# Kernel optimization log

Measured on AMD Instinct MI355X. Metric: run time of the kernel, lower is better.

## Reference

```python
import jax, jax.numpy as jnp
import numpy as np

B, T, D, K = 4, 4096, 1024, 64


def setup_inputs() -> dict:
    key = jax.random.key(0)
    k1, k2, k3, k4 = jax.random.split(key, 4)
    x = jax.random.normal(k1, (B, T, D), dtype=jnp.float32)
    Wq = jax.random.normal(k2, (D, K), dtype=jnp.float32) * (D ** -0.5)
    Wk = jax.random.normal(k3, (D, K), dtype=jnp.float32) * (D ** -0.5)
    Wv = jax.random.normal(k4, (D, D), dtype=jnp.float32) * (D ** -0.5)
    return {"x": x, "Wq": Wq, "Wk": Wk, "Wv": Wv}


def reference(x, Wq, Wk, Wv):
    # x: (B,T,D); single-head causal self-attention with value dim = D
    Bx, Tx, Dx = x.shape
    head_size = Wq.shape[-1]
    q = jnp.einsum('btd,dk->btk', x, Wq)  # (B,T,K)
    k = jnp.einsum('btd,dk->btk', x, Wk)  # (B,T,K)
    v = jnp.einsum('btd,de->bte', x, Wv)  # (B,T,D)
    scores = jnp.einsum('bqk,bsk->bqs', q, k) * (head_size ** -0.5)  # (B,T,T)
    causal = jnp.tril(jnp.ones((Tx, Tx), dtype=bool))
    scores = jnp.where(causal[None, :, :], scores, -jnp.inf)
    attn = jax.nn.softmax(scores, axis=-1)
    return jnp.einsum('bqs,bsd->bqd', attn, v)  # (B,T,D)
```

## Files before the change

kernel.cpp:

```cpp
#include <hip/hip_runtime.h>
#include <hip/hip_bf16.h>

typedef __attribute__((ext_vector_type(8))) short bf16x8;
typedef __attribute__((ext_vector_type(4))) float f32x4;
typedef unsigned short u16;

#define MFMA16(a, b, c) __builtin_amdgcn_mfma_f32_16x16x32_bf16((a), (b), (c), 0, 0, 0)
#define GLLDS(gp, lp)                                                                  \
  __builtin_amdgcn_global_load_lds((const __attribute__((address_space(1))) unsigned int*)(gp), \
                                   (__attribute__((address_space(3))) unsigned int*)(lp), 16, 0, 0)

__device__ __forceinline__ float fexp2(float x) { return __builtin_amdgcn_exp2f(x); }

__device__ __forceinline__ u16 f2b(float f) {
  union { float f; unsigned u; } x; x.f = f;
  return (u16)((x.u + 0x7FFFu + ((x.u >> 16) & 1u)) >> 16);
}
__device__ __forceinline__ unsigned f2b_hw(float f) {
  union { __hip_bfloat16 h; u16 u; } c;
  c.h = __float2bfloat16(f);
  return (unsigned)c.u;
}

__global__ __launch_bounds__(256) void k_cvt(const float* __restrict__ in,
                                             u16* __restrict__ out, int n4) {
  int i = blockIdx.x * 256 + threadIdx.x;
  if (i >= n4) return;
  float4 v = ((const float4*)in)[i];
  u16 a = f2b(v.x), b = f2b(v.y), c = f2b(v.z), d = f2b(v.w);
  ((uint2*)out)[i] = make_uint2((unsigned)a | ((unsigned)b << 16),
                                (unsigned)c | ((unsigned)d << 16));
}

__global__ __launch_bounds__(256) void k_packT(const float* __restrict__ in,
                                               u16* __restrict__ out, int R, int C) {
  __shared__ float t[32][33];
  int r0 = blockIdx.x * 32, c0 = blockIdx.y * 32;
  int cx = threadIdx.x & 31, ry = threadIdx.x >> 5;
#pragma unroll
  for (int k = 0; k < 4; k++)
    t[ry + k * 8][cx] = in[(size_t)(r0 + ry + k * 8) * C + c0 + cx];
  __syncthreads();
#pragma unroll
  for (int k = 0; k < 4; k++)
    out[(size_t)(c0 + ry + k * 8) * R + r0 + cx] = f2b(t[cx][ry + k * 8]);
}

__global__ __launch_bounds__(256) void k_gemm_qk(const u16* __restrict__ xb,
                                                 const u16* __restrict__ wqt,
                                                 const u16* __restrict__ wkt,
                                                 u16* __restrict__ q, u16* __restrict__ kk) {
  int row0 = blockIdx.x * 64;
  int tid = threadIdx.x, w = tid >> 6, l = tid & 63, l15 = l & 15, lg = l >> 4;
  const u16* wt = (w < 2) ? wqt : wkt;
  int nbase = (w & 1) * 32;
  f32x4 acc[4][2];
#pragma unroll
  for (int mt = 0; mt < 4; mt++)
#pragma unroll
    for (int nt = 0; nt < 2; nt++) acc[mt][nt] = (f32x4){0.f, 0.f, 0.f, 0.f};

  for (int k0 = 0; k0 < 1024; k0 += 32) {
    bf16x8 bfr[2], afr[4];
#pragma unroll
    for (int nt = 0; nt < 2; nt++)
      bfr[nt] = *(const bf16x8*)&wt[(size_t)(nbase + nt * 16 + l15) * 1024 + k0 + lg * 8];
#pragma unroll
    for (int mt = 0; mt < 4; mt++)
      afr[mt] = *(const bf16x8*)&xb[(size_t)(row0 + mt * 16 + l15) * 1024 + k0 + lg * 8];
#pragma unroll
    for (int mt = 0; mt < 4; mt++)
#pragma unroll
      for (int nt = 0; nt < 2; nt++) acc[mt][nt] = MFMA16(afr[mt], bfr[nt], acc[mt][nt]);
  }
  if (w < 2) {
#pragma unroll
    for (int mt = 0; mt < 4; mt++)
#pragma unroll
      for (int nt = 0; nt < 2; nt++)
#pragma unroll
        for (int j = 0; j < 4; j++)
          q[(size_t)(row0 + mt * 16 + lg * 4 + j) * 64 + nbase + nt * 16 + l15] =
              f2b(acc[mt][nt][j] * 0.18033688f);
  } else {
#pragma unroll
    for (int mt = 0; mt < 4; mt++)
#pragma unroll
      for (int nt = 0; nt < 2; nt++)
#pragma unroll
        for (int j = 0; j < 4; j++) {
          int row = row0 + mt * 16 + lg * 4 + j;
          int c = (nbase + nt * 16 + l15) * 2;
          size_t off = (size_t)(row >> 6) * 8192 + (row & 63) * 128 + (c ^ ((row & 7) << 4));
          *(u16*)((char*)kk + off) = f2b(acc[mt][nt][j]);
        }
  }
}

__global__ __launch_bounds__(256) void k_gemm_v(const u16* __restrict__ xb,
                                                const u16* __restrict__ wvt,
                                                u16* __restrict__ vT) {
  int b = blockIdx.z;
  int d0 = blockIdx.y * 128;
  int s0 = blockIdx.x * 128;
  int tid = threadIdx.x, w = tid >> 6, l = tid & 63, l15 = l & 15, lg = l >> 4;
  int wd = (w & 1) * 64, wsn = (w >> 1) * 64;
  __shared__ __align__(16) char lds[32768];

  const u16* arow = wvt + (size_t)d0 * 1024;
  const u16* brow = xb + (size_t)(b * 4096 + s0) * 1024;

  auto stage = [&](int buf, int k0) {
    char* La = lds + buf * 16384;
    char* Lb = La + 8192;
#pragma unroll
    for (int i = 0; i < 2; i++) {
      int row = w * 32 + i * 16 + (l >> 2), kq = (l & 3) * 8;
      GLLDS(&arow[(size_t)row * 1024 + k0 + kq], La + (w * 2 + i) * 1024);
      GLLDS(&brow[(size_t)row * 1024 + k0 + kq], Lb + (w * 2 + i) * 1024);
    }
  };

  f32x4 acc[4][4];
#pragma unroll
  for (int mt = 0; mt < 4; mt++)
#pragma unroll
    for (int nt = 0; nt < 4; nt++) acc[mt][nt] = (f32x4){0.f, 0.f, 0.f, 0.f};

  stage(0, 0);
  __syncthreads();
  int buf = 0;
  for (int k = 0; k < 32; k++) {
    if (k < 31) stage(buf ^ 1, (k + 1) * 32);
    const char* La = lds + buf * 16384;
    const char* Lb = La + 8192;
    bf16x8 afr[4], bfr[4];
#pragma unroll
    for (int mt = 0; mt < 4; mt++)
      afr[mt] = *(const bf16x8*)(La + (wd + mt * 16 + l15) * 64 + lg * 16);
#pragma unroll
    for (int nt = 0; nt < 4; nt++)
      bfr[nt] = *(const bf16x8*)(Lb + (wsn + nt * 16 + l15) * 64 + lg * 16);
    __builtin_amdgcn_s_setprio(1);
#pragma unroll
    for (int mt = 0; mt < 4; mt++)
#pragma unroll
      for (int nt = 0; nt < 4; nt++) acc[mt][nt] = MFMA16(afr[mt], bfr[nt], acc[mt][nt]);
    __builtin_amdgcn_s_setprio(0);
    __syncthreads();
    buf ^= 1;
  }
#pragma unroll
  for (int mt = 0; mt < 4; mt++)
#pragma unroll
    for (int nt = 0; nt < 4; nt++)
#pragma unroll
      for (int j = 0; j < 4; j++) {
        int d = d0 + wd + mt * 16 + lg * 4 + j;
        int s = s0 + wsn + nt * 16 + l15;
        size_t off = ((size_t)(b * 64 + (s >> 6)) * 8 + (d >> 7)) * 16384 + (d & 127) * 128 +
                     (((s & 63) * 2) ^ ((d & 7) << 4));
        *(u16*)((char*)vT + off) = f2b(acc[mt][nt][j]);
      }
}

__global__ __launch_bounds__(512, 2) void k_attn(const u16* __restrict__ qw,
                                                 const u16* __restrict__ kws,
                                                 const u16* __restrict__ vts,
                                                 float* __restrict__ out) {
  int bid = blockIdx.x;
  int xcd = bid & 7, r = bid >> 3;
  int cmb = r & 1, q5 = r >> 1;
  int half = q5 >> 4, idx = q5 & 15;
  int p = half ? 31 - idx : idx;
  int g = xcd * 2 + cmb;
  int cpair = g & 3, b = g >> 2;
  int tid = threadIdx.x, w = tid >> 6, l = tid & 63, l15 = l & 15, lg = l >> 4;
  int sw = (l15 & 7) << 4;
  size_t tokb = (size_t)b * 4096;

  __shared__ __align__(16) char lds[66048];
  char* Pb = lds + 49152;
  float* scb = (float*)(lds + 65536);

  const short ob = (short)0x3F80;
  const bf16x8 ones = {ob, ob, ob, ob, ob, ob, ob, ob};
  const bf16x8 zf = {0, 0, 0, 0, 0, 0, 0, 0};

  auto stageV = [&](int t) {
    const char* vb = (const char*)vts + ((size_t)(b * 64 + t) * 8 + cpair * 2) * 16384;
    char* lv = lds + 16384;
#pragma unroll
    for (int i = 0; i < 4; i++) {
      int s = w * 4 + i;
      GLLDS(vb + s * 1024 + l * 16, lv + s * 1024);
    }
  };
  auto stageK = [&](int t, int bufi) {
    const char* kb = (const char*)kws + (size_t)(b * 64 + t) * 8192;
    GLLDS(kb + w * 1024 + l * 16, lds + bufi * 8192 + w * 1024);
  };

  int Q0 = p * 128;
  int ntb = (Q0 >> 6) + 2;
  int qsA = Q0 + w * 16;
  int qA = qsA + l15;
  int qsB = Q0 + (w & 3) * 32;
  int dhalf = w >> 2;

  bf16x8 qf[2];
#pragma unroll
  for (int ks = 0; ks < 2; ks++)
    qf[ks] = *(const bf16x8*)&qw[(tokb + qA) * 64 + ks * 32 + lg * 8];

  f32x4 acc[8][2], accl[2];
  float mrow = -1e30f;
#pragma unroll
  for (int mt = 0; mt < 8; mt++)
#pragma unroll
    for (int qt = 0; qt < 2; qt++) acc[mt][qt] = (f32x4){0.f, 0.f, 0.f, 0.f};
  accl[0] = (f32x4){0.f, 0.f, 0.f, 0.f};
  accl[1] = (f32x4){0.f, 0.f, 0.f, 0.f};

  stageK(0, 0);
  __syncthreads();
  int buf = 0;
  for (int t = 0; t < ntb; t++) {
    int s0 = t * 64;
    stageV(t);
    if (t + 1 < ntb) stageK(t + 1, buf ^ 1);
    if (s0 < qsA + 16) {
      const char* Kb = lds + buf * 8192;
      f32x4 sfr[4];
      __builtin_amdgcn_s_setprio(1);
#pragma unroll
      for (int nt = 0; nt < 4; nt++) {
        const char* kr = Kb + (nt * 16 + l15) * 128;
        bf16x8 kf0 = *(const bf16x8*)(kr + ((lg * 16) ^ sw));
        bf16x8 kf1 = *(const bf16x8*)(kr + ((64 + lg * 16) ^ sw));
        f32x4 z = (f32x4){0.f, 0.f, 0.f, 0.f};
        z = MFMA16(kf0, qf[0], z);
        sfr[nt] = MFMA16(kf1, qf[1], z);
      }
      __builtin_amdgcn_s_setprio(0);
      if (s0 + 63 > qsA) {
#pragma unroll
        for (int nt = 0; nt < 4; nt++)
#pragma unroll
          for (int j = 0; j < 4; j++)
            if (s0 + nt * 16 + lg * 4 + j > qA) sfr[nt][j] = -1e30f;
      }
      float pm = fmaxf(fmaxf(fmaxf(sfr[0][0], sfr[0][1]), fmaxf(sfr[0][2], sfr[0][3])),
                       fmaxf(fmaxf(sfr[1][0], sfr[1][1]), fmaxf(sfr[1][2], sfr[1][3])));
      pm = fmaxf(pm, fmaxf(fmaxf(fmaxf(sfr[2][0], sfr[2][1]), fmaxf(sfr[2][2], sfr[2][3])),
                           fmaxf(fmaxf(sfr[3][0], sfr[3][1]), fmaxf(sfr[3][2], sfr[3][3]))));
      pm = fmaxf(pm, __shfl_xor(pm, 16));
      pm = fmaxf(pm, __shfl_xor(pm, 32));
      float sc = 1.0f;
      if (__any(pm > mrow + 11.54f)) {
        float mn = fmaxf(mrow, pm);
        sc = fexp2(mrow - mn);
        mrow = mn;
      }
      int rq = w * 16 + l15;
      scb[rq] = sc;
      int rbase = rq * 128, sx = (rq & 7) << 4;
#pragma unroll
      for (int nt = 0; nt < 4; nt++) {
        unsigned lo = f2b_hw(fexp2(sfr[nt][0] - mrow)) |
                      (f2b_hw(fexp2(sfr[nt][1] - mrow)) << 16);
        unsigned hi2 = f2b_hw(fexp2(sfr[nt][2] - mrow)) |
                       (f2b_hw(fexp2(sfr[nt][3] - mrow)) << 16);
        int addr = (rbase + (nt * 16 + lg * 4) * 2) ^ sx;
        *(uint2*)(Pb + addr) = make_uint2(lo, hi2);
      }
    }
    __syncthreads();
    if (s0 < qsB + 32) {
      const char* Vb = lds + 16384 + dhalf * 16384;
      bool act0 = s0 < qsB + 16;
      int R0 = (w & 3) * 32 + l15;
      if (act0) {
        float sq0 = scb[R0];
        if (!__all(sq0 == 1.0f)) {
#pragma unroll
          for (int mt = 0; mt < 8; mt++) acc[mt][0] *= sq0;
          accl[0] *= sq0;
        }
      }
      {
        float sq1 = scb[R0 + 16];
        if (!__all(sq1 == 1.0f)) {
#pragma unroll
          for (int mt = 0; mt < 8; mt++) acc[mt][1] *= sq1;
          accl[1] *= sq1;
        }
      }
      bf16x8 pf00 = zf, pf01 = zf, pf10, pf11;
      if (act0) {
        int rx = (R0 & 7) << 4;
        pf00 = *(const bf16x8*)(Pb + ((R0 * 128 + lg * 16) ^ rx));
        pf01 = *(const bf16x8*)(Pb + ((R0 * 128 + 64 + lg * 16) ^ rx));
      }
      {
        int R1 = R0 + 16, rx = (R1 & 7) << 4;
        pf10 = *(const bf16x8*)(Pb + ((R1 * 128 + lg * 16) ^ rx));
        pf11 = *(const bf16x8*)(Pb + ((R1 * 128 + 64 + lg * 16) ^ rx));
      }
      __builtin_amdgcn_s_setprio(1);
      accl[0] = MFMA16(ones, pf00, accl[0]);
      accl[0] = MFMA16(ones, pf01, accl[0]);
      accl[1] = MFMA16(ones, pf10, accl[1]);
      accl[1] = MFMA16(ones, pf11, accl[1]);
#pragma unroll
      for (int mt = 0; mt < 8; mt++) {
        const char* vr = Vb + (mt * 16 + l15) * 128;
        bf16x8 va0 = *(const bf16x8*)(vr + ((lg * 16) ^ sw));
        bf16x8 va1 = *(const bf16x8*)(vr + ((64 + lg * 16) ^ sw));
        acc[mt][0] = MFMA16(va0, pf00, acc[mt][0]);
        acc[mt][0] = MFMA16(va1, pf01, acc[mt][0]);
        acc[mt][1] = MFMA16(va0, pf10, acc[mt][1]);
        acc[mt][1] = MFMA16(va1, pf11, acc[mt][1]);
      }
      __builtin_amdgcn_s_setprio(0);
    }
    __syncthreads();
    buf ^= 1;
  }
#pragma unroll
  for (int qt = 0; qt < 2; qt++) {
    float linv = 1.0f / accl[qt][0];
#pragma unroll
    for (int mt = 0; mt < 8; mt++) {
      f32x4 v = acc[mt][qt] * linv;
      size_t o = (tokb + qsB + qt * 16 + l15) * 1024 + cpair * 256 + dhalf * 128 +
                 mt * 16 + lg * 4;
      *(f32x4*)&out[o] = v;
    }
  }
}

extern "C" void kernel_launch(void* const* d_in, const int* in_sizes, int n_in,
                              void* d_out, int out_size, void* d_ws, size_t ws_size,
                              hipStream_t stream) {
  const float* x  = (const float*)d_in[0];
  const float* Wq = (const float*)d_in[1];
  const float* Wk = (const float*)d_in[2];
  const float* Wv = (const float*)d_in[3];
  float* out = (float*)d_out;
  char* ws = (char*)d_ws;
  u16* xb  = (u16*)(ws);
  u16* qw  = (u16*)(ws + 33554432);
  u16* kw  = (u16*)(ws + 35651584);
  u16* vT  = (u16*)(ws + 37748736);
  u16* wqt = (u16*)(ws + 71303168);
  u16* wkt = (u16*)(ws + 71434240);
  u16* wvt = (u16*)(ws + 71565312);

  k_cvt<<<16384, 256, 0, stream>>>(x, xb, 4194304);
  k_packT<<<dim3(32, 2), 256, 0, stream>>>(Wq, wqt, 1024, 64);
  k_packT<<<dim3(32, 2), 256, 0, stream>>>(Wk, wkt, 1024, 64);
  k_packT<<<dim3(32, 32), 256, 0, stream>>>(Wv, wvt, 1024, 1024);
  k_gemm_qk<<<256, 256, 0, stream>>>(xb, wqt, wkt, qw, kw);
  k_gemm_v<<<dim3(32, 8, 4), 256, 0, stream>>>(xb, wvt, vT);
  k_attn<<<512, 512, 0, stream>>>(qw, kw, vT, out);
}
```

Baseline: 218.0 us.

## Load K fragments directly to registers and track softmax row sums in registers

```diff
diff --git a/kernel.cpp b/kernel.cpp
--- a/kernel.cpp
+++ b/kernel.cpp
@@ -179,26 +179,20 @@
   int sw = (l15 & 7) << 4;
   size_t tokb = (size_t)b * 4096;
 
-  __shared__ __align__(16) char lds[66048];
-  char* Pb = lds + 49152;
-  float* scb = (float*)(lds + 65536);
-
-  const short ob = (short)0x3F80;
-  const bf16x8 ones = {ob, ob, ob, ob, ob, ob, ob, ob};
+  __shared__ __align__(16) char lds[50176];
+  char* Pb = lds + 32768;
+  float* scb = (float*)(lds + 49152);
+  float* lb = (float*)(lds + 49664);
+
   const bf16x8 zf = {0, 0, 0, 0, 0, 0, 0, 0};
 
   auto stageV = [&](int t) {
     const char* vb = (const char*)vts + ((size_t)(b * 64 + t) * 8 + cpair * 2) * 16384;
-    char* lv = lds + 16384;
 #pragma unroll
     for (int i = 0; i < 4; i++) {
       int s = w * 4 + i;
-      GLLDS(vb + s * 1024 + l * 16, lv + s * 1024);
-    }
-  };
-  auto stageK = [&](int t, int bufi) {
-    const char* kb = (const char*)kws + (size_t)(b * 64 + t) * 8192;
-    GLLDS(kb + w * 1024 + l * 16, lds + bufi * 8192 + w * 1024);
+      GLLDS(vb + s * 1024 + l * 16, lds + s * 1024);
+    }
   };
 
   int Q0 = p * 128;
@@ -213,36 +207,47 @@
   for (int ks = 0; ks < 2; ks++)
     qf[ks] = *(const bf16x8*)&qw[(tokb + qA) * 64 + ks * 32 + lg * 8];
 
-  f32x4 acc[8][2], accl[2];
-  float mrow = -1e30f;
+  bf16x8 kf[4][2];
+  {
+    const char* kb = (const char*)kws + (size_t)(b * 64) * 8192;
+#pragma unroll
+    for (int nt = 0; nt < 4; nt++) {
+      const char* kr = kb + (nt * 16 + l15) * 128;
+      kf[nt][0] = *(const bf16x8*)(kr + ((lg * 16) ^ sw));
+      kf[nt][1] = *(const bf16x8*)(kr + ((64 + lg * 16) ^ sw));
+    }
+  }
+
+  f32x4 acc[8][2];
+  float mrow = -1e30f, Lrun = 0.f;
 #pragma unroll
   for (int mt = 0; mt < 8; mt++)
 #pragma unroll
     for (int qt = 0; qt < 2; qt++) acc[mt][qt] = (f32x4){0.f, 0.f, 0.f, 0.f};
-  accl[0] = (f32x4){0.f, 0.f, 0.f, 0.f};
-  accl[1] = (f32x4){0.f, 0.f, 0.f, 0.f};
-
-  stageK(0, 0);
-  __syncthreads();
-  int buf = 0;
+
   for (int t = 0; t < ntb; t++) {
     int s0 = t * 64;
     stageV(t);
-    if (t + 1 < ntb) stageK(t + 1, buf ^ 1);
     if (s0 < qsA + 16) {
-      const char* Kb = lds + buf * 8192;
       f32x4 sfr[4];
       __builtin_amdgcn_s_setprio(1);
 #pragma unroll
       for (int nt = 0; nt < 4; nt++) {
-        const char* kr = Kb + (nt * 16 + l15) * 128;
-        bf16x8 kf0 = *(const bf16x8*)(kr + ((lg * 16) ^ sw));
-        bf16x8 kf1 = *(const bf16x8*)(kr + ((64 + lg * 16) ^ sw));
         f32x4 z = (f32x4){0.f, 0.f, 0.f, 0.f};
-        z = MFMA16(kf0, qf[0], z);
-        sfr[nt] = MFMA16(kf1, qf[1], z);
+        z = MFMA16(kf[nt][0], qf[0], z);
+        sfr[nt] = MFMA16(kf[nt][1], qf[1], z);
       }
       __builtin_amdgcn_s_setprio(0);
+      {
+        int tn = (t + 1 < ntb) ? t + 1 : t;
+        const char* kbn = (const char*)kws + (size_t)(b * 64 + tn) * 8192;
+#pragma unroll
+        for (int nt = 0; nt < 4; nt++) {
+          const char* kr = kbn + (nt * 16 + l15) * 128;
+          kf[nt][0] = *(const bf16x8*)(kr + ((lg * 16) ^ sw));
+          kf[nt][1] = *(const bf16x8*)(kr + ((64 + lg * 16) ^ sw));
+        }
+      }
       if (s0 + 63 > qsA) {
 #pragma unroll
         for (int nt = 0; nt < 4; nt++)
@@ -265,19 +270,26 @@
       int rq = w * 16 + l15;
       scb[rq] = sc;
       int rbase = rq * 128, sx = (rq & 7) << 4;
+      float psum = 0.f;
 #pragma unroll
       for (int nt = 0; nt < 4; nt++) {
-        unsigned lo = f2b_hw(fexp2(sfr[nt][0] - mrow)) |
-                      (f2b_hw(fexp2(sfr[nt][1] - mrow)) << 16);
-        unsigned hi2 = f2b_hw(fexp2(sfr[nt][2] - mrow)) |
-                       (f2b_hw(fexp2(sfr[nt][3] - mrow)) << 16);
+        unsigned u0 = f2b_hw(fexp2(sfr[nt][0] - mrow));
+        unsigned u1 = f2b_hw(fexp2(sfr[nt][1] - mrow));
+        unsigned u2 = f2b_hw(fexp2(sfr[nt][2] - mrow));
+        unsigned u3 = f2b_hw(fexp2(sfr[nt][3] - mrow));
+        psum += __uint_as_float(u0 << 16) + __uint_as_float(u1 << 16) +
+                __uint_as_float(u2 << 16) + __uint_as_float(u3 << 16);
         int addr = (rbase + (nt * 16 + lg * 4) * 2) ^ sx;
-        *(uint2*)(Pb + addr) = make_uint2(lo, hi2);
-      }
+        *(uint2*)(Pb + addr) = make_uint2(u0 | (u1 << 16), u2 | (u3 << 16));
+      }
+      psum += __shfl_xor(psum, 16);
+      psum += __shfl_xor(psum, 32);
+      Lrun = Lrun * sc + psum;
+      if (lg == 0) lb[rq] = Lrun;
     }
     __syncthreads();
     if (s0 < qsB + 32) {
-      const char* Vb = lds + 16384 + dhalf * 16384;
+      const char* Vb = lds + dhalf * 16384;
       bool act0 = s0 < qsB + 16;
       int R0 = (w & 3) * 32 + l15;
       if (act0) {
@@ -285,7 +297,6 @@
         if (!__all(sq0 == 1.0f)) {
 #pragma unroll
           for (int mt = 0; mt < 8; mt++) acc[mt][0] *= sq0;
-          accl[0] *= sq0;
         }
       }
       {
@@ -293,7 +304,6 @@
         if (!__all(sq1 == 1.0f)) {
 #pragma unroll
           for (int mt = 0; mt < 8; mt++) acc[mt][1] *= sq1;
-          accl[1] *= sq1;
         }
       }
       bf16x8 pf00 = zf, pf01 = zf, pf10, pf11;
@@ -308,10 +318,6 @@
         pf11 = *(const bf16x8*)(Pb + ((R1 * 128 + 64 + lg * 16) ^ rx));
       }
       __builtin_amdgcn_s_setprio(1);
-      accl[0] = MFMA16(ones, pf00, accl[0]);
-      accl[0] = MFMA16(ones, pf01, accl[0]);
-      accl[1] = MFMA16(ones, pf10, accl[1]);
-      accl[1] = MFMA16(ones, pf11, accl[1]);
 #pragma unroll
       for (int mt = 0; mt < 8; mt++) {
         const char* vr = Vb + (mt * 16 + l15) * 128;
@@ -325,11 +331,10 @@
       __builtin_amdgcn_s_setprio(0);
     }
     __syncthreads();
-    buf ^= 1;
   }
 #pragma unroll
   for (int qt = 0; qt < 2; qt++) {
-    float linv = 1.0f / accl[qt][0];
+    float linv = 1.0f / lb[(w & 3) * 32 + qt * 16 + l15];
 #pragma unroll
     for (int mt = 0; mt < 8; mt++) {
       f32x4 v = acc[mt][qt] * linv;
```

Result: slower. 248.0 us (+13.7%).

## Retile PV stage to 64 queries x 64 dims per wave and track row sums in softmax

Applied to the files above, without the earlier changes.

```diff
diff --git a/kernel.cpp b/kernel.cpp
--- a/kernel.cpp
+++ b/kernel.cpp
@@ -179,13 +179,10 @@
   int sw = (l15 & 7) << 4;
   size_t tokb = (size_t)b * 4096;
 
-  __shared__ __align__(16) char lds[66048];
+  __shared__ __align__(16) char lds[66560];
   char* Pb = lds + 49152;
   float* scb = (float*)(lds + 65536);
-
-  const short ob = (short)0x3F80;
-  const bf16x8 ones = {ob, ob, ob, ob, ob, ob, ob, ob};
-  const bf16x8 zf = {0, 0, 0, 0, 0, 0, 0, 0};
+  float* lb = (float*)(lds + 66048);
 
   auto stageV = [&](int t) {
     const char* vb = (const char*)vts + ((size_t)(b * 64 + t) * 8 + cpair * 2) * 16384;
@@ -205,22 +202,20 @@
   int ntb = (Q0 >> 6) + 2;
   int qsA = Q0 + w * 16;
   int qA = qsA + l15;
-  int qsB = Q0 + (w & 3) * 32;
-  int dhalf = w >> 2;
+  int qpos = w & 1, dq = w >> 1;
+  int qsB = Q0 + qpos * 64;
 
   bf16x8 qf[2];
 #pragma unroll
   for (int ks = 0; ks < 2; ks++)
     qf[ks] = *(const bf16x8*)&qw[(tokb + qA) * 64 + ks * 32 + lg * 8];
 
-  f32x4 acc[8][2], accl[2];
-  float mrow = -1e30f;
-#pragma unroll
-  for (int mt = 0; mt < 8; mt++)
-#pragma unroll
-    for (int qt = 0; qt < 2; qt++) acc[mt][qt] = (f32x4){0.f, 0.f, 0.f, 0.f};
-  accl[0] = (f32x4){0.f, 0.f, 0.f, 0.f};
-  accl[1] = (f32x4){0.f, 0.f, 0.f, 0.f};
+  f32x4 acc[4][4];
+  float mrow = -1e30f, Lrun = 0.f;
+#pragma unroll
+  for (int mt = 0; mt < 4; mt++)
+#pragma unroll
+    for (int qt = 0; qt < 4; qt++) acc[mt][qt] = (f32x4){0.f, 0.f, 0.f, 0.f};
 
   stageK(0, 0);
   __syncthreads();
@@ -265,62 +260,55 @@
       int rq = w * 16 + l15;
       scb[rq] = sc;
       int rbase = rq * 128, sx = (rq & 7) << 4;
+      float psum = 0.f;
 #pragma unroll
       for (int nt = 0; nt < 4; nt++) {
-        unsigned lo = f2b_hw(fexp2(sfr[nt][0] - mrow)) |
-                      (f2b_hw(fexp2(sfr[nt][1] - mrow)) << 16);
-        unsigned hi2 = f2b_hw(fexp2(sfr[nt][2] - mrow)) |
-                       (f2b_hw(fexp2(sfr[nt][3] - mrow)) << 16);
+        unsigned u0 = f2b_hw(fexp2(sfr[nt][0] - mrow));
+        unsigned u1 = f2b_hw(fexp2(sfr[nt][1] - mrow));
+        unsigned u2 = f2b_hw(fexp2(sfr[nt][2] - mrow));
+        unsigned u3 = f2b_hw(fexp2(sfr[nt][3] - mrow));
+        psum += __uint_as_float(u0 << 16) + __uint_as_float(u1 << 16) +
+                __uint_as_float(u2 << 16) + __uint_as_float(u3 << 16);
         int addr = (rbase + (nt * 16 + lg * 4) * 2) ^ sx;
-        *(uint2*)(Pb + addr) = make_uint2(lo, hi2);
-      }
+        *(uint2*)(Pb + addr) = make_uint2(u0 | (u1 << 16), u2 | (u3 << 16));
+      }
+      psum += __shfl_xor(psum, 16);
+      psum += __shfl_xor(psum, 32);
+      Lrun = Lrun * sc + psum;
+      if (lg == 0) lb[rq] = Lrun;
     }
     __syncthreads();
-    if (s0 < qsB + 32) {
-      const char* Vb = lds + 16384 + dhalf * 16384;
-      bool act0 = s0 < qsB + 16;
-      int R0 = (w & 3) * 32 + l15;
-      if (act0) {
-        float sq0 = scb[R0];
-        if (!__all(sq0 == 1.0f)) {
-#pragma unroll
-          for (int mt = 0; mt < 8; mt++) acc[mt][0] *= sq0;
-          accl[0] *= sq0;
+    if (s0 < qsB + 64) {
+      int qlo = (s0 - qsB) >> 4;
+      if (qlo < 0) qlo = 0;
+      const char* Vb = lds + 16384 + (dq >> 1) * 16384;
+      int drow = (dq & 1) * 64;
+      bf16x8 pf[4][2];
+#pragma unroll
+      for (int qt = 0; qt < 4; qt++)
+        if (qt >= qlo) {
+          int R = qpos * 64 + qt * 16 + l15;
+          float sq = scb[R];
+          if (!__all(sq == 1.0f)) {
+#pragma unroll
+            for (int mt = 0; mt < 4; mt++) acc[mt][qt] *= sq;
+          }
+          int rx = (R & 7) << 4;
+          pf[qt][0] = *(const bf16x8*)(Pb + ((R * 128 + lg * 16) ^ rx));
+          pf[qt][1] = *(const bf16x8*)(Pb + ((R * 128 + 64 + lg * 16) ^ rx));
         }
-      }
-      {
-        float sq1 = scb[R0 + 16];
-        if (!__all(sq1 == 1.0f)) {
-#pragma unroll
-          for (int mt = 0; mt < 8; mt++) acc[mt][1] *= sq1;
-          accl[1] *= sq1;
-        }
-      }
-      bf16x8 pf00 = zf, pf01 = zf, pf10, pf11;
-      if (act0) {
-        int rx = (R0 & 7) << 4;
-        pf00 = *(const bf16x8*)(Pb + ((R0 * 128 + lg * 16) ^ rx));
-        pf01 = *(const bf16x8*)(Pb + ((R0 * 128 + 64 + lg * 16) ^ rx));
-      }
-      {
-        int R1 = R0 + 16, rx = (R1 & 7) << 4;
-        pf10 = *(const bf16x8*)(Pb + ((R1 * 128 + lg * 16) ^ rx));
-        pf11 = *(const bf16x8*)(Pb + ((R1 * 128 + 64 + lg * 16) ^ rx));
-      }
       __builtin_amdgcn_s_setprio(1);
-      accl[0] = MFMA16(ones, pf00, accl[0]);
-      accl[0] = MFMA16(ones, pf01, accl[0]);
-      accl[1] = MFMA16(ones, pf10, accl[1]);
-      accl[1] = MFMA16(ones, pf11, accl[1]);
-#pragma unroll
-      for (int mt = 0; mt < 8; mt++) {
-        const char* vr = Vb + (mt * 16 + l15) * 128;
+#pragma unroll
+      for (int mt = 0; mt < 4; mt++) {
+        const char* vr = Vb + (drow + mt * 16 + l15) * 128;
         bf16x8 va0 = *(const bf16x8*)(vr + ((lg * 16) ^ sw));
         bf16x8 va1 = *(const bf16x8*)(vr + ((64 + lg * 16) ^ sw));
-        acc[mt][0] = MFMA16(va0, pf00, acc[mt][0]);
-        acc[mt][0] = MFMA16(va1, pf01, acc[mt][0]);
-        acc[mt][1] = MFMA16(va0, pf10, acc[mt][1]);
-        acc[mt][1] = MFMA16(va1, pf11, acc[mt][1]);
+#pragma unroll
+        for (int qt = 0; qt < 4; qt++)
+          if (qt >= qlo) {
+            acc[mt][qt] = MFMA16(va0, pf[qt][0], acc[mt][qt]);
+            acc[mt][qt] = MFMA16(va1, pf[qt][1], acc[mt][qt]);
+          }
       }
       __builtin_amdgcn_s_setprio(0);
     }
@@ -328,12 +316,12 @@
     buf ^= 1;
   }
 #pragma unroll
-  for (int qt = 0; qt < 2; qt++) {
-    float linv = 1.0f / accl[qt][0];
-#pragma unroll
-    for (int mt = 0; mt < 8; mt++) {
+  for (int qt = 0; qt < 4; qt++) {
+    float linv = 1.0f / lb[qpos * 64 + qt * 16 + l15];
+#pragma unroll
+    for (int mt = 0; mt < 4; mt++) {
       f32x4 v = acc[mt][qt] * linv;
-      size_t o = (tokb + qsB + qt * 16 + l15) * 1024 + cpair * 256 + dhalf * 128 +
+      size_t o = (tokb + qsB + qt * 16 + l15) * 1024 + cpair * 256 + dq * 64 +
                  mt * 16 + lg * 4;
       *(f32x4*)&out[o] = v;
     }
```

After: 234.9 us. 7.7% more time.
